# Optimization experiments

Hardware: AMD Instinct MI355X
Metric: run time of the kernel (lower is better)

The kernel has to match this reference:

```python
import jax, jax.numpy as jnp
import numpy as np

DIM, NH, WS, SHIFT = 192, 6, 7, 3
HD = DIM // NH


def setup_inputs() -> dict:
    key = jax.random.key(0)
    ks = jax.random.split(key, 5)
    x = jax.random.normal(ks[0], (8, DIM, 224, 224), dtype=jnp.float32)
    s = 1.0 / np.sqrt(DIM)
    qkv_w = jax.random.normal(ks[1], (3 * DIM, DIM), dtype=jnp.float32) * s
    qkv_b = jnp.zeros((3 * DIM,), dtype=jnp.float32)
    proj_w = jax.random.normal(ks[2], (DIM, DIM), dtype=jnp.float32) * s
    proj_b = jnp.zeros((DIM,), dtype=jnp.float32)
    return {"x": x, "qkv_w": qkv_w, "qkv_b": qkv_b, "proj_w": proj_w, "proj_b": proj_b}


def reference(x, qkv_w, qkv_b, proj_w, proj_b):
    B, C, H, W = x.shape
    ws, nh, hd, shift = WS, NH, HD, SHIFT
    pad_h = (ws - H % ws) % ws
    pad_w = (ws - W % ws) % ws
    if pad_h or pad_w:
        x = jnp.pad(x, ((0, 0), (0, 0), (0, pad_h), (0, pad_w)))
    Hp, Wp = H + pad_h, W + pad_w
    if shift > 0:
        x = jnp.roll(x, (-shift, -shift), axis=(2, 3))
    # window partition: [B,C,Hp,Wp] -> [B*nWh*nWw, ws*ws, C]
    xw = (x.reshape(B, C, Hp // ws, ws, Wp // ws, ws)
           .transpose(0, 2, 4, 3, 5, 1)
           .reshape(-1, ws * ws, C))
    qkv = xw @ qkv_w.T + qkv_b                      # [N, 49, 3C]
    qkv = qkv.reshape(-1, ws * ws, 3, nh, hd).transpose(2, 0, 3, 1, 4)
    q, k, v = qkv[0], qkv[1], qkv[2]                # [N, nh, 49, hd]
    scale = hd ** (-0.5)
    attn = jnp.einsum('nhqd,nhkd->nhqk', q, k) * scale
    attn = jax.nn.softmax(attn, axis=-1)
    out = jnp.einsum('nhqk,nhkd->nhqd', attn, v)    # [N, nh, 49, hd]
    out = out.transpose(0, 2, 1, 3).reshape(-1, ws * ws, C)
    out = out @ proj_w.T + proj_b
    # window merge: [N, ws*ws, C] -> [B, C, Hp, Wp]
    out = (out.reshape(B, Hp // ws, Wp // ws, ws, ws, C)
              .transpose(0, 5, 1, 3, 2, 4)
              .reshape(B, C, Hp, Wp))
    if shift > 0:
        out = jnp.roll(out, (shift, shift), axis=(2, 3))
    return out[:, :, :H, :W]
```

## Files before the change

### kernel.cpp

```cpp
#include <hip/hip_runtime.h>
#include <hip/hip_fp16.h>

#define DIM   192
#define NH    6
#define WSZ   7
#define SHIFT 3
#define HD    32
#define TOK   49
#define HW    224
#define NWH   32
#define NWW   32
#define BATCH 8
#define NWIN  (BATCH*NWH*NWW)

typedef _Float16 half_t;
typedef _Float16 half8 __attribute__((ext_vector_type(8)));
typedef float    f32x4 __attribute__((ext_vector_type(4)));

#define WQKV_HALFS  (6*3*96*64)
#define WPROJ_HALFS (3*192*64)

__global__ __launch_bounds__(256) void prep_weights(const float* __restrict__ qkv_w,
                                                    const float* __restrict__ proj_w,
                                                    half_t* __restrict__ wp) {
  int e = blockIdx.x * 256 + threadIdx.x;
  if (e < WQKV_HALFS) {
    int h  = e / (3*96*64);
    int r1 = e % (3*96*64);
    int kc = r1 / (96*64);
    int r2 = r1 % (96*64);
    int r  = r2 / 64;
    int kl = r2 % 64;
    int g  = (r < 32) ? (h*32 + r) : (r < 64 ? (192 + h*32 + (r-32)) : (384 + h*32 + (r-64)));
    float v = qkv_w[g*192 + kc*64 + kl];
    int cs = (kl >> 3) ^ (r & 7);
    wp[((h*3 + kc)*96 + r)*64 + cs*8 + (kl & 7)] = (half_t)v;
  } else {
    int e2 = e - WQKV_HALFS;
    if (e2 < WPROJ_HALFS) {
      int kc = e2 / (192*64);
      int r2 = e2 % (192*64);
      int r  = r2 / 64;
      int kl = r2 % 64;
      float v = proj_w[r*192 + kc*64 + kl];
      int cs = (kl >> 3) ^ (r & 7);
      wp[WQKV_HALFS + (kc*192 + r)*64 + cs*8 + (kl & 7)] = (half_t)v;
    }
  }
}

#define OFF_XW 0
#define OFF_Q  20800
#define OFF_K  24960
#define OFF_VT 29120
#define OFF_AO 33216
#define OFF_W  54016
#define SMEM_BYTES 78592

__global__ __launch_bounds__(256, 2) void swin_attn(const float* __restrict__ x,
                                                    const float* __restrict__ qkv_b,
                                                    const float* __restrict__ proj_b,
                                                    const half_t* __restrict__ wp,
                                                    float* __restrict__ out) {
  __shared__ __align__(16) unsigned char smem[SMEM_BYTES];
  half_t* s_xw = (half_t*)(smem + OFF_XW);
  half_t* s_q  = (half_t*)(smem + OFF_Q);
  half_t* s_k  = (half_t*)(smem + OFF_K);
  half_t* s_vt = (half_t*)(smem + OFF_VT);
  half_t* s_ao = (half_t*)(smem + OFF_AO);
  half_t* s_w  = (half_t*)(smem + OFF_W);
  half_t* s_p  = (half_t*)(smem + OFF_W);
  float*  s_out= (float*)(smem);

  int bid = blockIdx.x;
  bid = (bid & 7) * 1024 + (bid >> 3);
  int b  = bid >> 10;
  int wh = (bid >> 5) & 31;
  int ww = bid & 31;

  int tid  = threadIdx.x;
  int wave = tid >> 6;
  int lane = tid & 63;
  int lg   = lane >> 4;
  int lr   = lane & 15;

  const float* xb = x + (size_t)b * DIM * HW * HW;

  for (int e = tid; e < TOK*DIM; e += 256) {
    int c = e / TOK;
    int r = e - c*TOK;
    int i = r / WSZ, j = r - i*WSZ;
    int hh = wh*WSZ + i + SHIFT; if (hh >= HW) hh -= HW;
    int wp2 = ww*WSZ + j + SHIFT; if (wp2 >= HW) wp2 -= HW;
    float v = xb[(size_t)c*HW*HW + hh*HW + wp2];
    s_xw[r*200 + c] = (half_t)v;
  }
  for (int e = tid; e < 300; e += 256)
    ((unsigned int*)(smem + OFF_XW + 49*400))[e] = 0u;
  __syncthreads();

  int mrow0 = wave * 16;
  const float qscale = 0.17677669529663687f;

  for (int h = 0; h < NH; ++h) {
    f32x4 acc[6];
    #pragma unroll
    for (int n = 0; n < 6; ++n) { acc[n][0]=0.f; acc[n][1]=0.f; acc[n][2]=0.f; acc[n][3]=0.f; }
    for (int kc = 0; kc < 3; ++kc) {
      {
        const uint4* src = (const uint4*)(wp + (size_t)(h*3 + kc)*96*64);
        uint4* dst = (uint4*)s_w;
        #pragma unroll
        for (int s = 0; s < 3; ++s) dst[tid + 256*s] = src[tid + 256*s];
      }
      __syncthreads();
      #pragma unroll
      for (int ks = 0; ks < 2; ++ks) {
        int kk = kc*64 + ks*32;
        half8 a = *(const half8*)(s_xw + (mrow0 + lr)*200 + kk + lg*8);
        #pragma unroll
        for (int n = 0; n < 6; ++n) {
          int rr = n*16 + lr;
          half8 bf = *(const half8*)(s_w + rr*64 + (((ks*4 + lg) ^ (rr & 7)) * 8));
          acc[n] = __builtin_amdgcn_mfma_f32_16x16x32_f16(a, bf, acc[n], 0, 0, 0);
        }
      }
      __syncthreads();
    }
    #pragma unroll
    for (int n = 0; n < 6; ++n) {
      int sect = n >> 1;
      int chl  = (n & 1)*16 + lr;
      int gch  = (sect == 0) ? (h*32 + chl) : (sect == 1 ? (192 + h*32 + chl) : (384 + h*32 + chl));
      float bia = qkv_b[gch];
      if (sect < 2) {
        #pragma unroll
        for (int jj = 0; jj < 4; ++jj) {
          int tok = mrow0 + lg*4 + jj;
          if (tok < 52) {
            float v = acc[n][jj] + bia;
            if (sect == 0) v *= qscale;
            (sect == 0 ? s_q : s_k)[tok*40 + chl] = (half_t)v;
          }
        }
      } else {
        int tok0 = mrow0 + lg*4;
        union { half_t hh4[4]; uint2 u; } pk;
        #pragma unroll
        for (int jj = 0; jj < 4; ++jj) {
          int tok = tok0 + jj;
          float v = (tok < TOK) ? (acc[n][jj] + bia) : 0.f;
          pk.hh4[jj] = (half_t)v;
        }
        int chunk = (tok0 >> 3) ^ (chl & 7);
        *(uint2*)(s_vt + chl*64 + chunk*8 + (tok0 & 7)) = pk.u;
      }
    }
    __syncthreads();

    f32x4 sacc[4];
    #pragma unroll
    for (int n = 0; n < 4; ++n) { sacc[n][0]=0.f; sacc[n][1]=0.f; sacc[n][2]=0.f; sacc[n][3]=0.f; }
    {
      half8 a = *(const half8*)(s_q + (mrow0 + lr)*40 + lg*8);
      #pragma unroll
      for (int n = 0; n < 4; ++n) {
        half8 bf = *(const half8*)(s_k + (n*16 + lr)*40 + lg*8);
        sacc[n] = __builtin_amdgcn_mfma_f32_16x16x32_f16(a, bf, sacc[n], 0, 0, 0);
      }
    }
    if (lr >= 1) {
      #pragma unroll
      for (int jj = 0; jj < 4; ++jj) sacc[3][jj] = -1e30f;
    }
    float rl[4];
    #pragma unroll
    for (int jj = 0; jj < 4; ++jj) {
      float m = fmaxf(fmaxf(sacc[0][jj], sacc[1][jj]), fmaxf(sacc[2][jj], sacc[3][jj]));
      #pragma unroll
      for (int d = 1; d < 16; d <<= 1) m = fmaxf(m, __shfl_xor(m, d));
      float p[4], ssum = 0.f;
      #pragma unroll
      for (int n = 0; n < 4; ++n) { p[n] = __expf(sacc[n][jj] - m); ssum += p[n]; }
      #pragma unroll
      for (int d = 1; d < 16; d <<= 1) ssum += __shfl_xor(ssum, d);
      rl[jj] = 1.f / ssum;
      int tok = mrow0 + lg*4 + jj;
      if (tok < 52) {
        #pragma unroll
        for (int n = 0; n < 4; ++n)
          s_p[tok*72 + n*16 + lr] = (half_t)p[n];
      }
    }
    __syncthreads();

    f32x4 oacc[2];
    oacc[0][0]=0.f; oacc[0][1]=0.f; oacc[0][2]=0.f; oacc[0][3]=0.f;
    oacc[1][0]=0.f; oacc[1][1]=0.f; oacc[1][2]=0.f; oacc[1][3]=0.f;
    #pragma unroll
    for (int ks = 0; ks < 2; ++ks) {
      half8 a = *(const half8*)(s_p + (mrow0 + lr)*72 + ks*32 + lg*8);
      #pragma unroll
      for (int n = 0; n < 2; ++n) {
        int d = n*16 + lr;
        int chunk = (ks*4 + lg) ^ (d & 7);
        half8 bf = *(const half8*)(s_vt + d*64 + chunk*8);
        oacc[n] = __builtin_amdgcn_mfma_f32_16x16x32_f16(a, bf, oacc[n], 0, 0, 0);
      }
    }
    #pragma unroll
    for (int n = 0; n < 2; ++n) {
      #pragma unroll
      for (int jj = 0; jj < 4; ++jj) {
        int tok = mrow0 + lg*4 + jj;
        if (tok < 52)
          s_ao[tok*200 + h*32 + n*16 + lr] = (half_t)(oacc[n][jj] * rl[jj]);
      }
    }
    __syncthreads();
  }

  f32x4 pacc[12];
  #pragma unroll
  for (int n = 0; n < 12; ++n) { pacc[n][0]=0.f; pacc[n][1]=0.f; pacc[n][2]=0.f; pacc[n][3]=0.f; }
  for (int kc = 0; kc < 3; ++kc) {
    {
      const uint4* src = (const uint4*)(wp + WQKV_HALFS + (size_t)kc*192*64);
      uint4* dst = (uint4*)s_w;
      #pragma unroll
      for (int s = 0; s < 6; ++s) dst[tid + 256*s] = src[tid + 256*s];
    }
    __syncthreads();
    #pragma unroll
    for (int ks = 0; ks < 2; ++ks) {
      int kk = kc*64 + ks*32;
      half8 a = *(const half8*)(s_ao + (mrow0 + lr)*200 + kk + lg*8);
      #pragma unroll
      for (int n = 0; n < 12; ++n) {
        int rr = n*16 + lr;
        half8 bf = *(const half8*)(s_w + rr*64 + (((ks*4 + lg) ^ (rr & 7)) * 8));
        pacc[n] = __builtin_amdgcn_mfma_f32_16x16x32_f16(a, bf, pacc[n], 0, 0, 0);
      }
    }
    __syncthreads();
  }
  #pragma unroll
  for (int n = 0; n < 12; ++n) {
    int ch = n*16 + lr;
    float bia = proj_b[ch];
    #pragma unroll
    for (int jj = 0; jj < 4; ++jj) {
      int tok = mrow0 + lg*4 + jj;
      if (tok < TOK) s_out[ch*52 + tok] = pacc[n][jj] + bia;
    }
  }
  __syncthreads();
  float* ob = out + (size_t)b * DIM * HW * HW;
  for (int e = tid; e < TOK*DIM; e += 256) {
    int c = e / TOK;
    int r = e - c*TOK;
    int i = r / WSZ, j = r - i*WSZ;
    int hh = wh*WSZ + i + SHIFT; if (hh >= HW) hh -= HW;
    int wp2 = ww*WSZ + j + SHIFT; if (wp2 >= HW) wp2 -= HW;
    ob[(size_t)c*HW*HW + hh*HW + wp2] = s_out[c*52 + r];
  }
}

extern "C" void kernel_launch(void* const* d_in, const int* in_sizes, int n_in,
                              void* d_out, int out_size, void* d_ws, size_t ws_size,
                              hipStream_t stream) {
  const float* x      = (const float*)d_in[0];
  const float* qkv_w  = (const float*)d_in[1];
  const float* qkv_b  = (const float*)d_in[2];
  const float* proj_w = (const float*)d_in[3];
  const float* proj_b = (const float*)d_in[4];
  half_t* wpk = (half_t*)d_ws;

  prep_weights<<<576, 256, 0, stream>>>(qkv_w, proj_w, wpk);
  swin_attn<<<NWIN, 256, 0, stream>>>(x, qkv_b, proj_b, wpk, (float*)d_out);
}
```

Baseline: 859.6 us.

## Split each window across 8 waves and fuse projection per head

```diff
diff --git a/kernel.cpp b/kernel.cpp
--- a/kernel.cpp
+++ b/kernel.cpp
@@ -5,20 +5,16 @@
 #define NH    6
 #define WSZ   7
 #define SHIFT 3
-#define HD    32
 #define TOK   49
 #define HW    224
-#define NWH   32
-#define NWW   32
-#define BATCH 8
-#define NWIN  (BATCH*NWH*NWW)
+#define NWIN  8192
 
 typedef _Float16 half_t;
 typedef _Float16 half8 __attribute__((ext_vector_type(8)));
 typedef float    f32x4 __attribute__((ext_vector_type(4)));
 
 #define WQKV_HALFS  (6*3*96*64)
-#define WPROJ_HALFS (3*192*64)
+#define WPROJ_HALFS (6*192*32)
 
 __global__ __launch_bounds__(256) void prep_weights(const float* __restrict__ qkv_w,
                                                     const float* __restrict__ proj_w,
@@ -38,39 +34,36 @@
   } else {
     int e2 = e - WQKV_HALFS;
     if (e2 < WPROJ_HALFS) {
-      int kc = e2 / (192*64);
-      int r2 = e2 % (192*64);
-      int r  = r2 / 64;
-      int kl = r2 % 64;
-      float v = proj_w[r*192 + kc*64 + kl];
-      int cs = (kl >> 3) ^ (r & 7);
-      wp[WQKV_HALFS + (kc*192 + r)*64 + cs*8 + (kl & 7)] = (half_t)v;
+      int h  = e2 / (192*32);
+      int r  = (e2 >> 5) % 192;
+      int kl = e2 & 31;
+      wp[WQKV_HALFS + e2] = (half_t)proj_w[r*192 + h*32 + kl];
     }
   }
 }
 
-#define OFF_XW 0
-#define OFF_Q  20800
-#define OFF_K  24960
-#define OFF_VT 29120
-#define OFF_AO 33216
-#define OFF_W  54016
-#define SMEM_BYTES 78592
-
-__global__ __launch_bounds__(256, 2) void swin_attn(const float* __restrict__ x,
+#define OFF_X   0
+#define OFF_Q   19600
+#define OFF_K   23760
+#define OFF_VT  27920
+#define OFF_AOH 32016
+#define OFF_W   36176
+#define SMEM_BYTES 48464
+
+__global__ __launch_bounds__(512, 4) void swin_attn(const float* __restrict__ x,
                                                     const float* __restrict__ qkv_b,
                                                     const float* __restrict__ proj_b,
                                                     const half_t* __restrict__ wp,
                                                     float* __restrict__ out) {
   __shared__ __align__(16) unsigned char smem[SMEM_BYTES];
-  half_t* s_xw = (half_t*)(smem + OFF_XW);
-  half_t* s_q  = (half_t*)(smem + OFF_Q);
-  half_t* s_k  = (half_t*)(smem + OFF_K);
-  half_t* s_vt = (half_t*)(smem + OFF_VT);
-  half_t* s_ao = (half_t*)(smem + OFF_AO);
-  half_t* s_w  = (half_t*)(smem + OFF_W);
-  half_t* s_p  = (half_t*)(smem + OFF_W);
-  float*  s_out= (float*)(smem);
+  half_t* s_x   = (half_t*)(smem + OFF_X);
+  half_t* s_q   = (half_t*)(smem + OFF_Q);
+  half_t* s_k   = (half_t*)(smem + OFF_K);
+  half_t* s_vt  = (half_t*)(smem + OFF_VT);
+  half_t* s_aoh = (half_t*)(smem + OFF_AOH);
+  half_t* s_w   = (half_t*)(smem + OFF_W);
+  half_t* s_p   = (half_t*)(smem + OFF_W);
+  float*  s_out = (float*)(smem);
 
   int bid = blockIdx.x;
   bid = (bid & 7) * 1024 + (bid >> 3);
@@ -83,77 +76,94 @@
   int lane = tid & 63;
   int lg   = lane >> 4;
   int lr   = lane & 15;
+  int m    = wave & 3;
+  int nh   = wave >> 2;
+  int mrow0 = m * 16;
 
   const float* xb = x + (size_t)b * DIM * HW * HW;
 
-  for (int e = tid; e < TOK*DIM; e += 256) {
+  for (int e = tid; e < TOK*DIM; e += 512) {
     int c = e / TOK;
     int r = e - c*TOK;
     int i = r / WSZ, j = r - i*WSZ;
     int hh = wh*WSZ + i + SHIFT; if (hh >= HW) hh -= HW;
     int wp2 = ww*WSZ + j + SHIFT; if (wp2 >= HW) wp2 -= HW;
-    float v = xb[(size_t)c*HW*HW + hh*HW + wp2];
-    s_xw[r*200 + c] = (half_t)v;
-  }
-  for (int e = tid; e < 300; e += 256)
-    ((unsigned int*)(smem + OFF_XW + 49*400))[e] = 0u;
-  __syncthreads();
-
-  int mrow0 = wave * 16;
+    s_x[r*200 + c] = (half_t)xb[(size_t)c*HW*HW + hh*HW + wp2];
+  }
+
+  f32x4 pacc[6];
+  #pragma unroll
+  for (int n = 0; n < 6; ++n) { pacc[n][0]=0.f; pacc[n][1]=0.f; pacc[n][2]=0.f; pacc[n][3]=0.f; }
+
   const float qscale = 0.17677669529663687f;
+  const half_t* wproj = wp + WQKV_HALFS;
+  const half8 ZERO8 = {0,0,0,0,0,0,0,0};
+  const uint4* wsrc = (const uint4*)wp;
+
+  uint4 r0 = wsrc[tid], r1;
+  if (tid < 256) r1 = wsrc[512 + tid];
 
   for (int h = 0; h < NH; ++h) {
-    f32x4 acc[6];
-    #pragma unroll
-    for (int n = 0; n < 6; ++n) { acc[n][0]=0.f; acc[n][1]=0.f; acc[n][2]=0.f; acc[n][3]=0.f; }
+    f32x4 acc[3];
+    #pragma unroll
+    for (int n = 0; n < 3; ++n) { acc[n][0]=0.f; acc[n][1]=0.f; acc[n][2]=0.f; acc[n][3]=0.f; }
     for (int kc = 0; kc < 3; ++kc) {
+      int cidx = h*3 + kc;
+      __syncthreads();
       {
-        const uint4* src = (const uint4*)(wp + (size_t)(h*3 + kc)*96*64);
         uint4* dst = (uint4*)s_w;
-        #pragma unroll
-        for (int s = 0; s < 3; ++s) dst[tid + 256*s] = src[tid + 256*s];
+        dst[tid] = r0;
+        if (tid < 256) dst[512 + tid] = r1;
+        if (cidx < 17) {
+          const uint4* nx = wsrc + (size_t)(cidx + 1) * 768;
+          r0 = nx[tid];
+          if (tid < 256) r1 = nx[512 + tid];
+        }
       }
       __syncthreads();
       #pragma unroll
       for (int ks = 0; ks < 2; ++ks) {
-        int kk = kc*64 + ks*32;
-        half8 a = *(const half8*)(s_xw + (mrow0 + lr)*200 + kk + lg*8);
-        #pragma unroll
-        for (int n = 0; n < 6; ++n) {
-          int rr = n*16 + lr;
+        int row = mrow0 + lr;
+        int rowc = row > 48 ? 48 : row;
+        half8 a = *(const half8*)(s_x + rowc*200 + kc*64 + ks*32 + lg*8);
+        if (row > 48) a = ZERO8;
+        #pragma unroll
+        for (int i = 0; i < 3; ++i) {
+          int rr = (nh*3 + i)*16 + lr;
           half8 bf = *(const half8*)(s_w + rr*64 + (((ks*4 + lg) ^ (rr & 7)) * 8));
-          acc[n] = __builtin_amdgcn_mfma_f32_16x16x32_f16(a, bf, acc[n], 0, 0, 0);
-        }
-      }
-      __syncthreads();
-    }
-    #pragma unroll
-    for (int n = 0; n < 6; ++n) {
-      int sect = n >> 1;
-      int chl  = (n & 1)*16 + lr;
-      int gch  = (sect == 0) ? (h*32 + chl) : (sect == 1 ? (192 + h*32 + chl) : (384 + h*32 + chl));
-      float bia = qkv_b[gch];
-      if (sect < 2) {
+          acc[i] = __builtin_amdgcn_mfma_f32_16x16x32_f16(a, bf, acc[i], 0, 0, 0);
+        }
+      }
+    }
+    #pragma unroll
+    for (int i = 0; i < 3; ++i) {
+      int nt   = nh*3 + i;
+      int sect = nt >> 1;
+      int chl  = (nt & 1)*16 + lr;
+      float bia = qkv_b[sect*192 + h*32 + chl];
+      if (sect == 0) {
         #pragma unroll
         for (int jj = 0; jj < 4; ++jj) {
           int tok = mrow0 + lg*4 + jj;
-          if (tok < 52) {
-            float v = acc[n][jj] + bia;
-            if (sect == 0) v *= qscale;
-            (sect == 0 ? s_q : s_k)[tok*40 + chl] = (half_t)v;
-          }
+          if (tok < 52) s_q[tok*40 + chl] = (half_t)((acc[i][jj] + bia) * qscale);
+        }
+      } else if (sect == 1) {
+        #pragma unroll
+        for (int jj = 0; jj < 4; ++jj) {
+          int tok = mrow0 + lg*4 + jj;
+          if (tok < 52) s_k[tok*40 + chl] = (half_t)(acc[i][jj] + bia);
         }
       } else {
         int tok0 = mrow0 + lg*4;
-        union { half_t hh4[4]; uint2 u; } pk;
+        union { half_t h4[4]; uint2 u; } pk2;
         #pragma unroll
         for (int jj = 0; jj < 4; ++jj) {
           int tok = tok0 + jj;
-          float v = (tok < TOK) ? (acc[n][jj] + bia) : 0.f;
-          pk.hh4[jj] = (half_t)v;
+          float v = (tok < TOK) ? (acc[i][jj] + bia) : 0.f;
+          pk2.h4[jj] = (half_t)v;
         }
         int chunk = (tok0 >> 3) ^ (chl & 7);
-        *(uint2*)(s_vt + chl*64 + chunk*8 + (tok0 & 7)) = pk.u;
+        *(uint2*)(s_vt + chl*64 + chunk*8 + (tok0 & 7)) = pk2.u;
       }
     }
     __syncthreads();
@@ -176,87 +186,68 @@
     float rl[4];
     #pragma unroll
     for (int jj = 0; jj < 4; ++jj) {
-      float m = fmaxf(fmaxf(sacc[0][jj], sacc[1][jj]), fmaxf(sacc[2][jj], sacc[3][jj]));
-      #pragma unroll
-      for (int d = 1; d < 16; d <<= 1) m = fmaxf(m, __shfl_xor(m, d));
+      float mx = fmaxf(fmaxf(sacc[0][jj], sacc[1][jj]), fmaxf(sacc[2][jj], sacc[3][jj]));
+      #pragma unroll
+      for (int d = 1; d < 16; d <<= 1) mx = fmaxf(mx, __shfl_xor(mx, d));
       float p[4], ssum = 0.f;
       #pragma unroll
-      for (int n = 0; n < 4; ++n) { p[n] = __expf(sacc[n][jj] - m); ssum += p[n]; }
+      for (int n = 0; n < 4; ++n) { p[n] = __expf(sacc[n][jj] - mx); ssum += p[n]; }
       #pragma unroll
       for (int d = 1; d < 16; d <<= 1) ssum += __shfl_xor(ssum, d);
       rl[jj] = 1.f / ssum;
-      int tok = mrow0 + lg*4 + jj;
-      if (tok < 52) {
-        #pragma unroll
-        for (int n = 0; n < 4; ++n)
-          s_p[tok*72 + n*16 + lr] = (half_t)p[n];
+      if (nh == 0) {
+        int tok = mrow0 + lg*4 + jj;
+        if (tok < 52) {
+          #pragma unroll
+          for (int n = 0; n < 4; ++n)
+            s_p[tok*72 + n*16 + lr] = (half_t)p[n];
+        }
       }
     }
     __syncthreads();
 
-    f32x4 oacc[2];
-    oacc[0][0]=0.f; oacc[0][1]=0.f; oacc[0][2]=0.f; oacc[0][3]=0.f;
-    oacc[1][0]=0.f; oacc[1][1]=0.f; oacc[1][2]=0.f; oacc[1][3]=0.f;
+    f32x4 oacc;
+    oacc[0]=0.f; oacc[1]=0.f; oacc[2]=0.f; oacc[3]=0.f;
     #pragma unroll
     for (int ks = 0; ks < 2; ++ks) {
       half8 a = *(const half8*)(s_p + (mrow0 + lr)*72 + ks*32 + lg*8);
-      #pragma unroll
-      for (int n = 0; n < 2; ++n) {
-        int d = n*16 + lr;
-        int chunk = (ks*4 + lg) ^ (d & 7);
-        half8 bf = *(const half8*)(s_vt + d*64 + chunk*8);
-        oacc[n] = __builtin_amdgcn_mfma_f32_16x16x32_f16(a, bf, oacc[n], 0, 0, 0);
-      }
-    }
-    #pragma unroll
-    for (int n = 0; n < 2; ++n) {
-      #pragma unroll
-      for (int jj = 0; jj < 4; ++jj) {
-        int tok = mrow0 + lg*4 + jj;
-        if (tok < 52)
-          s_ao[tok*200 + h*32 + n*16 + lr] = (half_t)(oacc[n][jj] * rl[jj]);
-      }
-    }
-    __syncthreads();
-  }
-
-  f32x4 pacc[12];
-  #pragma unroll
-  for (int n = 0; n < 12; ++n) { pacc[n][0]=0.f; pacc[n][1]=0.f; pacc[n][2]=0.f; pacc[n][3]=0.f; }
-  for (int kc = 0; kc < 3; ++kc) {
-    {
-      const uint4* src = (const uint4*)(wp + WQKV_HALFS + (size_t)kc*192*64);
-      uint4* dst = (uint4*)s_w;
-      #pragma unroll
-      for (int s = 0; s < 6; ++s) dst[tid + 256*s] = src[tid + 256*s];
-    }
-    __syncthreads();
-    #pragma unroll
-    for (int ks = 0; ks < 2; ++ks) {
-      int kk = kc*64 + ks*32;
-      half8 a = *(const half8*)(s_ao + (mrow0 + lr)*200 + kk + lg*8);
-      #pragma unroll
-      for (int n = 0; n < 12; ++n) {
-        int rr = n*16 + lr;
-        half8 bf = *(const half8*)(s_w + rr*64 + (((ks*4 + lg) ^ (rr & 7)) * 8));
-        pacc[n] = __builtin_amdgcn_mfma_f32_16x16x32_f16(a, bf, pacc[n], 0, 0, 0);
-      }
-    }
-    __syncthreads();
-  }
-  #pragma unroll
-  for (int n = 0; n < 12; ++n) {
-    int ch = n*16 + lr;
-    float bia = proj_b[ch];
+      int d = nh*16 + lr;
+      int chunk = (ks*4 + lg) ^ (d & 7);
+      half8 bf = *(const half8*)(s_vt + d*64 + chunk*8);
+      oacc = __builtin_amdgcn_mfma_f32_16x16x32_f16(a, bf, oacc, 0, 0, 0);
+    }
     #pragma unroll
     for (int jj = 0; jj < 4; ++jj) {
       int tok = mrow0 + lg*4 + jj;
-      if (tok < TOK) s_out[ch*52 + tok] = pacc[n][jj] + bia;
+      if (tok < 52) s_aoh[tok*40 + nh*16 + lr] = (half_t)(oacc[jj] * rl[jj]);
+    }
+    __syncthreads();
+
+    {
+      half8 a = *(const half8*)(s_aoh + (mrow0 + lr)*40 + lg*8);
+      #pragma unroll
+      for (int i2 = 0; i2 < 6; ++i2) {
+        int ch = (nh*6 + i2)*16 + lr;
+        half8 bf = *(const half8*)(wproj + ((size_t)h*192 + ch)*32 + lg*8);
+        pacc[i2] = __builtin_amdgcn_mfma_f32_16x16x32_f16(a, bf, pacc[i2], 0, 0, 0);
+      }
+    }
+  }
+  __syncthreads();
+
+  #pragma unroll
+  for (int i2 = 0; i2 < 6; ++i2) {
+    int ch = (nh*6 + i2)*16 + lr;
+    float bia = proj_b[ch];
+    #pragma unroll
+    for (int jj = 0; jj < 4; ++jj) {
+      int tok = mrow0 + lg*4 + jj;
+      if (tok < TOK) s_out[ch*52 + tok] = pacc[i2][jj] + bia;
     }
   }
   __syncthreads();
   float* ob = out + (size_t)b * DIM * HW * HW;
-  for (int e = tid; e < TOK*DIM; e += 256) {
+  for (int e = tid; e < TOK*DIM; e += 512) {
     int c = e / TOK;
     int r = e - c*TOK;
     int i = r / WSZ, j = r - i*WSZ;
@@ -277,5 +268,5 @@
   half_t* wpk = (half_t*)d_ws;
 
   prep_weights<<<576, 256, 0, stream>>>(qkv_w, proj_w, wpk);
-  swin_attn<<<NWIN, 256, 0, stream>>>(x, qkv_b, proj_b, wpk, (float*)d_out);
+  swin_attn<<<NWIN, 512, 0, stream>>>(x, qkv_b, proj_b, wpk, (float*)d_out);
 }
```

Result: faster. 739.8 us (-13.9%).
